# Kernel optimization log

Hardware: AMD Instinct MI355X
Metric: run time of the kernel (lower is better)

## Reference

```python
import jax, jax.numpy as jnp
import numpy as np

D_MODEL, D_STATE, D_CONV, D_INNER = 1024, 16, 4, 2048
BATCH, SEQ = 4, 2048


def silu(v):
    return v * jax.nn.sigmoid(v)


def setup_inputs() -> dict:
    key = jax.random.key(0)
    ks = jax.random.split(key, 7)
    x = jax.random.normal(ks[0], (BATCH, SEQ, D_MODEL), dtype=jnp.float32)
    s = 0.02
    W_in = jax.random.normal(ks[1], (D_MODEL, 2 * D_INNER), dtype=jnp.float32) * s
    conv_w = jax.random.normal(ks[2], (D_INNER, 1, D_CONV), dtype=jnp.float32) * s  # depthwise (O, I/g=1, K)
    conv_b = jax.random.normal(ks[3], (D_INNER,), dtype=jnp.float32) * s
    W_xproj = jax.random.normal(ks[4], (D_INNER, 2 * D_STATE + 1), dtype=jnp.float32) * s
    A_log = jnp.log(jnp.tile(jnp.arange(1, D_STATE + 1, dtype=jnp.float32), (D_INNER, 1)))
    D = jnp.ones((D_INNER,), dtype=jnp.float32)
    W_out = jax.random.normal(ks[5], (D_INNER, D_MODEL), dtype=jnp.float32) * s
    return {"x": x, "W_in": W_in, "conv_w": conv_w, "conv_b": conv_b,
            "W_xproj": W_xproj, "A_log": A_log, "D": D, "W_out": W_out}


def reference(x, W_in, conv_w, conv_b, W_xproj, A_log, D, W_out):
    B, L, _ = x.shape
    xz = x @ W_in                                   # (B, L, 2*d_inner)
    x_proj, z = jnp.split(xz, 2, axis=-1)
    # Depthwise causal conv: padding=d_conv-1 then truncate to L == left-pad only.
    xc = jax.lax.conv_general_dilated(
        x_proj.transpose(0, 2, 1), conv_w,
        window_strides=(1,), padding=[(D_CONV - 1, 0)],
        feature_group_count=D_INNER,
        dimension_numbers=("NCH", "OIH", "NCH"))
    x_conv = silu((xc + conv_b[None, :, None]).transpose(0, 2, 1))  # (B, L, d_inner)
    ssm = x_conv @ W_xproj                           # (B, L, 1+2*d_state)
    delta = jax.nn.softplus(ssm[..., 0])             # (B, L)
    Bm = ssm[..., 1:1 + D_STATE]                     # (B, L, d_state)
    Cm = ssm[..., 1 + D_STATE:]                      # (B, L, d_state)
    # Original: deltaA = exp(delta*A) and softmax weights are computed but unused.
    deltaB = delta[..., None] * Bm                   # (B, L, d_state)
    # h_approx = mean_L(x outer deltaB): avoid (B,L,d_inner,d_state) intermediate.
    h_mean = jnp.einsum("bld,bln->bdn", x_conv, deltaB) / L  # (B, d_inner, d_state)
    y = jnp.einsum("bdn,bln->bld", h_mean, Cm)       # (B, L, d_inner)
    y = y + D[None, None, :] * x_conv
    y = y * silu(z)
    return y @ W_out                                 # (B, L, d_model)
```

## Files before the change

### kernel.cpp

```cpp
#include <hip/hip_runtime.h>
#include <hip/hip_bf16.h>
#include <stdint.h>

typedef __bf16 bf16x8 __attribute__((ext_vector_type(8)));
typedef float f32x4 __attribute__((ext_vector_type(4)));
typedef float f32x2 __attribute__((ext_vector_type(2)));
typedef unsigned short u16;
typedef u16 ushort2v __attribute__((ext_vector_type(2)));
typedef u16 ushort4v __attribute__((ext_vector_type(4)));
typedef u16 ushort8v __attribute__((ext_vector_type(8)));

__device__ __forceinline__ u16 f2bf(float f) {
    union { float f; uint32_t u; } v; v.f = f;
    uint32_t u = v.u + 0x7FFFu + ((v.u >> 16) & 1u);
    return (u16)(u >> 16);
}
__device__ __forceinline__ float bf2f(u16 b) {
    union { uint32_t u; float f; } v; v.u = ((uint32_t)b) << 16;
    return v.f;
}
__device__ __forceinline__ float silu_f(float v) {
    return v / (1.0f + __expf(-v));
}
__device__ __forceinline__ void gload_lds16(const u16* g, u16* l) {
    __builtin_amdgcn_global_load_lds(
        (const __attribute__((address_space(1))) void*)g,
        (__attribute__((address_space(3))) void*)l, 16, 0, 0);
}

__device__ __forceinline__ void trans_tile(
        const float* __restrict__ src, u16* __restrict__ dst, int R, int C,
        int bc, int br, float (*tt)[33], int tid) {
    const int tx = tid & 31, ty = tid >> 5;
#pragma unroll
    for (int i = 0; i < 4; i++)
        tt[ty + i * 8][tx] = src[(int64_t)(br * 32 + ty + i * 8) * C + bc * 32 + tx];
    __syncthreads();
    const int wx = tid & 15, wy = tid >> 4;
#pragma unroll
    for (int i = 0; i < 2; i++) {
        int c = wy + i * 16;
        ushort2v o = { f2bf(tt[wx * 2][c]), f2bf(tt[wx * 2 + 1][c]) };
        *(ushort2v*)&dst[(int64_t)(bc * 32 + c) * R + br * 32 + wx * 2] = o;
    }
}

__global__ __launch_bounds__(256) void prep_k(
        const float* __restrict__ x, u16* __restrict__ x_bf,
        const float* __restrict__ Wi, u16* __restrict__ Wti,
        const float* __restrict__ Wo, u16* __restrict__ Wto,
        const float* __restrict__ wx, u16* __restrict__ wxt) {
    __shared__ float tt[32][33];
    const int blk = blockIdx.x, tid = threadIdx.x;
    if (blk < 4096) {
        int64_t i = ((int64_t)blk * 256 + tid) * 8;
        float4 v0 = *(const float4*)&x[i];
        float4 v1 = *(const float4*)&x[i + 4];
        ushort8v o = { f2bf(v0.x), f2bf(v0.y), f2bf(v0.z), f2bf(v0.w),
                       f2bf(v1.x), f2bf(v1.y), f2bf(v1.z), f2bf(v1.w) };
        *(ushort8v*)&x_bf[i] = o;
    } else if (blk < 8192) {
        int t = blk - 4096;
        trans_tile(Wi, Wti, 1024, 4096, t & 127, t >> 7, tt, tid);
    } else if (blk < 10240) {
        int t = blk - 8192;
        trans_tile(Wo, Wto, 2048, 1024, t & 31, t >> 5, tt, tid);
    } else {
        int idx = (blk - 10240) * 256 + tid;
        int j = idx >> 11, d = idx & 2047;
        wxt[idx] = (j < 33) ? f2bf(wx[d * 33 + j]) : (u16)0;
    }
}

template<int M_REP, int WARPS_M, int B_HALVES, bool OUT_BF16>
__global__ __launch_bounds__(512) void gemm_dp(
        const u16* __restrict__ A, const u16* __restrict__ Bt,
        void* __restrict__ Cout, int nbn_sh, int NT, int lda, int ldb, int ldc) {
    constexpr int WARPS_N = 8 / WARPS_M;
    constexpr int QPT = M_REP / 2;
    constexpr int WV_M = M_REP * 16;
    constexpr int BN = WARPS_N * 64;
    constexpr int B_T = BN * 64;

    __shared__ __align__(16) u16 As[2 * 16384];
    __shared__ __align__(16) u16 Bs[2 * B_T];

    const int tid = threadIdx.x;
    const int wave = tid >> 6;
    const int lane = tid & 63;
    const int wm = wave / WARPS_N, wn = wave % WARPS_N;
    const int fr = lane & 15, fq = lane >> 4;

    const int nwg = gridDim.x;
    const int cpx = nwg >> 3;
    const int swz = (blockIdx.x & 7) * cpx + (blockIdx.x >> 3);
    const int bm = swz >> nbn_sh;
    const int bn = swz & ((1 << nbn_sh) - 1);

    const int srow = tid >> 3;
    const int scol8 = ((tid & 7) ^ (srow & 7)) * 8;
    const u16* gA = A + (int64_t)(bm * 256 + srow) * lda + scol8;
    const u16* gB = Bt + (int64_t)(bn * BN + srow) * ldb + scol8;
    const int64_t lda64 = lda, ldb64 = ldb;

    const int ksw0 = ((fq) ^ (fr & 7)) * 8;
    const int ksw1 = ((4 + fq) ^ (fr & 7)) * 8;
    const int arow0 = (wm * WV_M + fr) * 64;
    const int brow0 = (wn * 64 + fr) * 64;

    auto STAGE_A_HALF = [&](int kt, int buf, int h) {
#pragma unroll
        for (int j = 0; j < 2; ++j)
            gload_lds16(gA + (int64_t)(h * 128 + j * 64) * lda64 + kt * 64,
                        &As[buf * 16384 + h * 8192 + j * 4096 + tid * 8]);
    };
    auto STAGE_B_HALF = [&](int kt, int buf, int h) {
#pragma unroll
        for (int j = 0; j < 2; ++j)
            gload_lds16(gB + (int64_t)(h * 128 + j * 64) * ldb64 + kt * 64,
                        &Bs[buf * B_T + h * 8192 + j * 4096 + tid * 8]);
    };

    f32x4 acc[M_REP][4] = {};

    STAGE_A_HALF(0, 0, 0); STAGE_A_HALF(0, 0, 1);
#pragma unroll
    for (int h = 0; h < B_HALVES; ++h) STAGE_B_HALF(0, 0, h);
#pragma unroll
    for (int h = 0; h < B_HALVES; ++h) STAGE_B_HALF(1, 1, h);
    if constexpr (B_HALVES == 2) { asm volatile("s_waitcnt vmcnt(4)" ::: "memory"); }
    else                         { asm volatile("s_waitcnt vmcnt(2)" ::: "memory"); }
    __builtin_amdgcn_s_barrier();

    const int NI = NT >> 1;
    for (int s = 0; s < NI; ++s) {
        const bool more = (s + 1 < NI);
#pragma unroll
        for (int t = 0; t < 2; ++t) {
            const u16* Ab = &As[t * 16384];
            const u16* Bb = &Bs[t * B_T];
            bf16x8 breg[4][2];
            bf16x8 areg[2][2][2];
#pragma unroll
            for (int q = 0; q < QPT; ++q) {
                const int p = q & 1;
                if (q == 0) {
#pragma unroll
                    for (int n = 0; n < 4; ++n) {
                        breg[n][0] = *(const bf16x8*)(Bb + brow0 + n * 1024 + ksw0);
                        breg[n][1] = *(const bf16x8*)(Bb + brow0 + n * 1024 + ksw1);
                    }
#pragma unroll
                    for (int j = 0; j < 2; ++j) {
                        areg[0][j][0] = *(const bf16x8*)(Ab + arow0 + j * 1024 + ksw0);
                        areg[0][j][1] = *(const bf16x8*)(Ab + arow0 + j * 1024 + ksw1);
                    }
                }
                __builtin_amdgcn_s_setprio(1);
                if (q + 1 < QPT) {
#pragma unroll
                    for (int j = 0; j < 2; ++j) {
                        areg[p ^ 1][j][0] = *(const bf16x8*)(Ab + arow0 + (2 * (q + 1) + j) * 1024 + ksw0);
                        areg[p ^ 1][j][1] = *(const bf16x8*)(Ab + arow0 + (2 * (q + 1) + j) * 1024 + ksw1);
                    }
                }
#pragma unroll
                for (int j = 0; j < 2; ++j)
#pragma unroll
                    for (int n = 0; n < 4; ++n) {
                        acc[2 * q + j][n] = __builtin_amdgcn_mfma_f32_16x16x32_bf16(
                            areg[p][j][0], breg[n][0], acc[2 * q + j][n], 0, 0, 0);
                        acc[2 * q + j][n] = __builtin_amdgcn_mfma_f32_16x16x32_bf16(
                            areg[p][j][1], breg[n][1], acc[2 * q + j][n], 0, 0, 0);
                    }
                if (q + 1 < QPT) {
#pragma unroll
                    for (int g = 0; g < 4; ++g) {
                        __builtin_amdgcn_sched_group_barrier(0x008, 2, 0);
                        __builtin_amdgcn_sched_group_barrier(0x100, 1, 0);
                        __builtin_amdgcn_sched_group_barrier(0x008, 2, 0);
                    }
                }
                __builtin_amdgcn_s_setprio(0);
                if constexpr (QPT == 4) {
                    if (t == 0 && q == 0)         STAGE_A_HALF(2 * s + 1, 1, 0);
                    if (t == 0 && q == 1)         STAGE_A_HALF(2 * s + 1, 1, 1);
                    if (t == 0 && q == 2 && more) STAGE_B_HALF(2 * s + 2, 0, 0);
                    if (t == 0 && q == 3 && more) STAGE_B_HALF(2 * s + 2, 0, 1);
                    if (t == 1 && q == 0 && more) STAGE_A_HALF(2 * s + 2, 0, 0);
                    if (t == 1 && q == 1 && more) STAGE_A_HALF(2 * s + 2, 0, 1);
                    if (t == 1 && q == 2 && more) STAGE_B_HALF(2 * s + 3, 1, 0);
                    if (t == 1 && q == 3 && more) STAGE_B_HALF(2 * s + 3, 1, 1);
                } else {
                    if (t == 0 && q == 0)         STAGE_A_HALF(2 * s + 1, 1, 0);
                    if (t == 0 && q == 1) {       STAGE_A_HALF(2 * s + 1, 1, 1);
                        if (more)                 STAGE_B_HALF(2 * s + 2, 0, 0); }
                    if (t == 1 && q == 0 && more) STAGE_A_HALF(2 * s + 2, 0, 0);
                    if (t == 1 && q == 1 && more) { STAGE_A_HALF(2 * s + 2, 0, 1);
                                                    STAGE_B_HALF(2 * s + 3, 1, 0); }
                }
                if (q == QPT - 1) {
                    if (more) {
                        if constexpr (B_HALVES == 2) { asm volatile("s_waitcnt vmcnt(4)" ::: "memory"); }
                        else                         { asm volatile("s_waitcnt vmcnt(2)" ::: "memory"); }
                    } else {
                        asm volatile("s_waitcnt vmcnt(0)" ::: "memory");
                    }
                }
                __builtin_amdgcn_s_barrier();
            }
        }
    }

#pragma unroll
    for (int m = 0; m < M_REP; ++m) {
#pragma unroll
        for (int n = 0; n < 4; ++n) {
            const int col = bn * BN + wn * 64 + n * 16 + fr;
#pragma unroll
            for (int r = 0; r < 4; ++r) {
                const int row = bm * 256 + wm * WV_M + m * 16 + fq * 4 + r;
                if constexpr (OUT_BF16)
                    ((u16*)Cout)[(int64_t)row * ldc + col] = f2bf(acc[m][n][r]);
                else
                    ((float*)Cout)[(int64_t)row * ldc + col] = acc[m][n][r];
            }
        }
    }
}

__global__ __launch_bounds__(256) void gemm3_k(
        const u16* __restrict__ A, const u16* __restrict__ Bt,
        float* __restrict__ Cout, int NT, int lda, int ldb, int ldc) {
    __shared__ __align__(16) u16 As[2 * 8192];
    __shared__ __align__(16) u16 Bs[2 * 8192];

    const int tid = threadIdx.x;
    const int wave = tid >> 6;
    const int lane = tid & 63;
    const int wm = wave >> 1, wn = wave & 1;
    const int fr = lane & 15, fq = lane >> 4;

    const int nwg = gridDim.x;
    const int cpx = nwg >> 3;
    const int swz = (blockIdx.x & 7) * cpx + (blockIdx.x >> 3);
    const int bm = swz >> 3;
    const int bn = swz & 7;

    const int srow = tid >> 3;
    const int scol8 = ((tid & 7) ^ (srow & 7)) * 8;
    const u16* gA = A + (int64_t)(bm * 128 + srow) * lda + scol8;
    const u16* gB = Bt + (int64_t)(bn * 128 + srow) * ldb + scol8;
    const int64_t lda64 = lda, ldb64 = ldb;

    const int ksw0 = ((fq) ^ (fr & 7)) * 8;
    const int ksw1 = ((4 + fq) ^ (fr & 7)) * 8;
    const int arow0 = (wm * 64 + fr) * 64;
    const int brow0 = (wn * 64 + fr) * 64;

    auto STAGE_A = [&](int kt, int buf, int h) {
#pragma unroll
        for (int j = 0; j < 2; ++j)
            gload_lds16(gA + (int64_t)(h * 64 + j * 32) * lda64 + kt * 64,
                        &As[buf * 8192 + h * 4096 + j * 2048 + tid * 8]);
    };
    auto STAGE_B = [&](int kt, int buf, int h) {
#pragma unroll
        for (int j = 0; j < 2; ++j)
            gload_lds16(gB + (int64_t)(h * 64 + j * 32) * ldb64 + kt * 64,
                        &Bs[buf * 8192 + h * 4096 + j * 2048 + tid * 8]);
    };

    f32x4 acc[4][4] = {};

    STAGE_A(0, 0, 0); STAGE_A(0, 0, 1);
    STAGE_B(0, 0, 0); STAGE_B(0, 0, 1);
    STAGE_B(1, 1, 0); STAGE_B(1, 1, 1);
    asm volatile("s_waitcnt vmcnt(4)" ::: "memory");
    __builtin_amdgcn_s_barrier();

    for (int t = 0; t < NT; ++t) {
        const u16* Ab = &As[(t & 1) * 8192];
        const u16* Bb = &Bs[(t & 1) * 8192];
        bf16x8 breg[4][2];
        bf16x8 areg[2][2][2];
#pragma unroll
        for (int n = 0; n < 4; ++n) {
            breg[n][0] = *(const bf16x8*)(Bb + brow0 + n * 1024 + ksw0);
            breg[n][1] = *(const bf16x8*)(Bb + brow0 + n * 1024 + ksw1);
        }
#pragma unroll
        for (int j = 0; j < 2; ++j) {
            areg[0][j][0] = *(const bf16x8*)(Ab + arow0 + j * 1024 + ksw0);
            areg[0][j][1] = *(const bf16x8*)(Ab + arow0 + j * 1024 + ksw1);
        }
        if (t + 1 < NT) STAGE_A(t + 1, (t + 1) & 1, 0);
        __builtin_amdgcn_s_barrier();
        asm volatile("s_waitcnt lgkmcnt(0)" ::: "memory");
        __builtin_amdgcn_sched_barrier(0);
        __builtin_amdgcn_s_setprio(1);
#pragma unroll
        for (int j = 0; j < 2; ++j) {
            areg[1][j][0] = *(const bf16x8*)(Ab + arow0 + (2 + j) * 1024 + ksw0);
            areg[1][j][1] = *(const bf16x8*)(Ab + arow0 + (2 + j) * 1024 + ksw1);
        }
#pragma unroll
        for (int j = 0; j < 2; ++j)
#pragma unroll
            for (int n = 0; n < 4; ++n) {
                acc[j][n] = __builtin_amdgcn_mfma_f32_16x16x32_bf16(
                    areg[0][j][0], breg[n][0], acc[j][n], 0, 0, 0);
                acc[j][n] = __builtin_amdgcn_mfma_f32_16x16x32_bf16(
                    areg[0][j][1], breg[n][1], acc[j][n], 0, 0, 0);
            }
#pragma unroll
        for (int g = 0; g < 4; ++g) {
            __builtin_amdgcn_sched_group_barrier(0x008, 2, 0);
            __builtin_amdgcn_sched_group_barrier(0x100, 1, 0);
            __builtin_amdgcn_sched_group_barrier(0x008, 2, 0);
        }
        __builtin_amdgcn_s_setprio(0);
        __builtin_amdgcn_s_barrier();
        if (t + 1 < NT) STAGE_A(t + 1, (t + 1) & 1, 1);
        if (t + 2 < NT) { STAGE_B(t + 2, t & 1, 0); STAGE_B(t + 2, t & 1, 1); }
        __builtin_amdgcn_s_barrier();
        asm volatile("s_waitcnt lgkmcnt(0)" ::: "memory");
        __builtin_amdgcn_sched_barrier(0);
        __builtin_amdgcn_s_setprio(1);
#pragma unroll
        for (int j = 0; j < 2; ++j)
#pragma unroll
            for (int n = 0; n < 4; ++n) {
                acc[2 + j][n] = __builtin_amdgcn_mfma_f32_16x16x32_bf16(
                    areg[1][j][0], breg[n][0], acc[2 + j][n], 0, 0, 0);
                acc[2 + j][n] = __builtin_amdgcn_mfma_f32_16x16x32_bf16(
                    areg[1][j][1], breg[n][1], acc[2 + j][n], 0, 0, 0);
            }
        __builtin_amdgcn_s_setprio(0);
        if (t + 2 < NT) { asm volatile("s_waitcnt vmcnt(4)" ::: "memory"); }
        else            { asm volatile("s_waitcnt vmcnt(0)" ::: "memory"); }
        __builtin_amdgcn_s_barrier();
    }

#pragma unroll
    for (int m = 0; m < 4; ++m) {
#pragma unroll
        for (int n = 0; n < 4; ++n) {
            const int col = bn * 128 + wn * 64 + n * 16 + fr;
#pragma unroll
            for (int r = 0; r < 4; ++r) {
                const int row = bm * 128 + wm * 64 + m * 16 + fq * 4 + r;
                Cout[(int64_t)row * ldc + col] = acc[m][n][r];
            }
        }
    }
}

__global__ __launch_bounds__(256) void conv_ssm_k(
        const u16* __restrict__ xz, const float* __restrict__ cw,
        const float* __restrict__ cb, const u16* __restrict__ wxt,
        u16* __restrict__ xc, float* __restrict__ dB, float* __restrict__ Cm) {
    __shared__ __align__(16) u16 Xs[16][2064];
    __shared__ float Sred[4][16][48];
    __shared__ float deltas[16];
    const int blk = blockIdx.x;
    const int b = blk >> 7, lb = blk & 127;
    const int l0 = lb << 4;
    const int64_t r0 = (int64_t)b * 2048 + l0;
    const int tid = threadIdx.x;
    const int d0 = tid * 8;

    float w[8][4], bias[8];
#pragma unroll
    for (int j = 0; j < 8; j++) {
        float4 wv = *(const float4*)&cw[(d0 + j) * 4];
        w[j][0] = wv.x; w[j][1] = wv.y; w[j][2] = wv.z; w[j][3] = wv.w;
        bias[j] = cb[d0 + j];
    }
    float win[4][8];
#pragma unroll
    for (int r = 0; r < 3; r++) {
        int l = l0 - 3 + r;
        if (l < 0) {
#pragma unroll
            for (int j = 0; j < 8; j++) win[r][j] = 0.f;
        } else {
            ushort8v v = *(const ushort8v*)&xz[((int64_t)b * 2048 + l) * 4096 + d0];
#pragma unroll
            for (int j = 0; j < 8; j++) win[r][j] = bf2f(v[j]);
        }
    }
    ushort8v rows[16];
#pragma unroll
    for (int li = 0; li < 16; li++)
        rows[li] = *(const ushort8v*)&xz[(r0 + li) * 4096 + d0];

#pragma unroll
    for (int li = 0; li < 16; li++) {
#pragma unroll
        for (int j = 0; j < 8; j++) win[(3 + li) & 3][j] = bf2f(rows[li][j]);
        ushort8v o;
#pragma unroll
        for (int j = 0; j < 8; j++) {
            float s = bias[j];
#pragma unroll
            for (int k = 0; k < 4; k++) s += w[j][k] * win[(li + k) & 3][j];
            o[j] = f2bf(silu_f(s));
        }
        *(ushort8v*)&xc[(r0 + li) * 2048 + d0] = o;
        *(ushort8v*)&Xs[li][d0] = o;
    }
    __syncthreads();

    const int kc = tid >> 6;
    const int lane = tid & 63;
    const int fr = lane & 15, fq = lane >> 4;
    const u16* bp = wxt + (int64_t)fr * 2048 + kc * 512 + fq * 8;
    const u16* ap = &Xs[fr][kc * 512 + fq * 8];
    f32x4 acc0 = {}, acc1 = {}, acc2 = {};
#pragma unroll 4
    for (int k = 0; k < 512; k += 32) {
        bf16x8 av = *(const bf16x8*)(ap + k);
        bf16x8 b0 = *(const bf16x8*)(bp + k);
        bf16x8 b1 = *(const bf16x8*)(bp + 16 * 2048 + k);
        bf16x8 b2 = *(const bf16x8*)(bp + 32 * 2048 + k);
        acc0 = __builtin_amdgcn_mfma_f32_16x16x32_bf16(av, b0, acc0, 0, 0, 0);
        acc1 = __builtin_amdgcn_mfma_f32_16x16x32_bf16(av, b1, acc1, 0, 0, 0);
        acc2 = __builtin_amdgcn_mfma_f32_16x16x32_bf16(av, b2, acc2, 0, 0, 0);
    }
#pragma unroll
    for (int r = 0; r < 4; r++) {
        Sred[kc][fq * 4 + r][fr]      = acc0[r];
        Sred[kc][fq * 4 + r][16 + fr] = acc1[r];
        Sred[kc][fq * 4 + r][32 + fr] = acc2[r];
    }
    __syncthreads();
    if (tid < 16) {
        float s0 = Sred[0][tid][0] + Sred[1][tid][0] + Sred[2][tid][0] + Sred[3][tid][0];
        deltas[tid] = (s0 > 20.f) ? s0 : log1pf(__expf(s0));
    }
    __syncthreads();
    {
        const int row = tid >> 4, n = tid & 15;
        float sB = Sred[0][row][1 + n] + Sred[1][row][1 + n] +
                   Sred[2][row][1 + n] + Sred[3][row][1 + n];
        float sC = Sred[0][row][17 + n] + Sred[1][row][17 + n] +
                   Sred[2][row][17 + n] + Sred[3][row][17 + n];
        dB[(r0 + row) * 16 + n] = deltas[row] * sB * (1.0f / 2048.0f);
        Cm[(r0 + row) * 16 + n] = sC;
    }
}

__global__ __launch_bounds__(256) void h_part_k(
        const u16* __restrict__ xc, const float* __restrict__ dB,
        float* __restrict__ hp) {
    const int blk = blockIdx.x;
    const int dt = blk & 3, b = (blk >> 2) & 3, lc = blk >> 4;
    const int d = dt * 512 + threadIdx.x * 2;
    const u16* xp = xc + ((int64_t)(b * 2048 + lc * 64)) * 2048 + d;
    const f32x2* dbp = (const f32x2*)(dB + (int64_t)(b * 2048 + lc * 64) * 16);
    f32x2 acc0[8] = {}, acc1[8] = {};
    for (int l = 0; l < 64; l++) {
        ushort2v xv = *(const ushort2v*)&xp[(int64_t)l * 2048];
        float x0 = bf2f(xv[0]), x1 = bf2f(xv[1]);
#pragma unroll
        for (int q = 0; q < 8; q++) {
            f32x2 dv = dbp[l * 8 + q];
            acc0[q] += dv * x0;
            acc1[q] += dv * x1;
        }
    }
    float* o = hp + ((int64_t)((lc * 4 + b) * 2048 + d)) * 16;
#pragma unroll
    for (int q = 0; q < 8; q++) *(f32x2*)&o[q * 2] = acc0[q];
#pragma unroll
    for (int q = 0; q < 8; q++) *(f32x2*)&o[16 + q * 2] = acc1[q];
}

__global__ void h_red_k(const float* __restrict__ hp, float* __restrict__ h) {
    const int i4 = blockIdx.x * 256 + threadIdx.x;
    f32x4 s = {};
#pragma unroll
    for (int c = 0; c < 32; c++)
        s += *(const f32x4*)&hp[(int64_t)c * 131072 + i4 * 4];
    *(f32x4*)&h[i4 * 4] = s;
}

__global__ __launch_bounds__(256) void y_gate_k(
        u16* __restrict__ xz, const u16* __restrict__ xc,
        const float* __restrict__ h, const float* __restrict__ Cm,
        const float* __restrict__ Dp) {
    const int blk = blockIdx.x;
    const int lc = blk & 127, b = blk >> 7;
    const int d0 = threadIdx.x * 8;
    const float* hpp = h + ((int64_t)(b * 2048 + d0)) * 16;
    float hreg[8][16];
#pragma unroll
    for (int i = 0; i < 8; i++)
#pragma unroll
        for (int n4 = 0; n4 < 4; n4++) {
            f32x4 hv = *(const f32x4*)&hpp[i * 16 + n4 * 4];
            hreg[i][n4 * 4 + 0] = hv[0]; hreg[i][n4 * 4 + 1] = hv[1];
            hreg[i][n4 * 4 + 2] = hv[2]; hreg[i][n4 * 4 + 3] = hv[3];
        }
    float Dv[8];
    {
        f32x4 dv0 = *(const f32x4*)&Dp[d0];
        f32x4 dv1 = *(const f32x4*)&Dp[d0 + 4];
#pragma unroll
        for (int i = 0; i < 4; i++) { Dv[i] = dv0[i]; Dv[4 + i] = dv1[i]; }
    }
    __shared__ float Cs[16][16];
    if (threadIdx.x < 64)
        ((float4*)&Cs[0][0])[threadIdx.x] =
            ((const float4*)(Cm + (int64_t)(b * 2048 + lc * 16) * 16))[threadIdx.x];
    __syncthreads();
#pragma unroll 4
    for (int li = 0; li < 16; li++) {
        const int64_t rowz = (int64_t)(b * 2048 + lc * 16 + li);
        ushort8v xcv = *(const ushort8v*)&xc[rowz * 2048 + d0];
        ushort8v zv = *(const ushort8v*)&xz[rowz * 4096 + 2048 + d0];
        ushort8v o;
#pragma unroll
        for (int i = 0; i < 8; i++) {
            float s = Dv[i] * bf2f(xcv[i]);
#pragma unroll
            for (int n = 0; n < 16; n++) s += hreg[i][n] * Cs[li][n];
            o[i] = f2bf(s * silu_f(bf2f(zv[i])));
        }
        *(ushort8v*)&xz[rowz * 4096 + d0] = o;
    }
}

extern "C" void kernel_launch(void* const* d_in, const int* in_sizes, int n_in,
                              void* d_out, int out_size, void* d_ws, size_t ws_size,
                              hipStream_t stream) {
    (void)in_sizes; (void)n_in; (void)out_size; (void)ws_size;
    const float* x      = (const float*)d_in[0];
    const float* W_in   = (const float*)d_in[1];
    const float* conv_w = (const float*)d_in[2];
    const float* conv_b = (const float*)d_in[3];
    const float* W_xp   = (const float*)d_in[4];
    const float* Dp     = (const float*)d_in[6];
    const float* W_out  = (const float*)d_in[7];
    float* out = (float*)d_out;
    char* ws = (char*)d_ws;

    u16*   x_bf   = (u16*)(ws);
    float* dB     = (float*)(ws);
    float* Cm     = (float*)(ws + 524288);
    float* h      = (float*)(ws + 1048576);
    float* hp     = (float*)(ws + 1572864);
    u16*   Wt_in  = (u16*)(ws + 16777216);
    u16*   Wt_out = (u16*)(ws + 25165824);
    u16*   Wxt    = (u16*)(ws + 29360128);
    u16*   xz     = (u16*)(ws + 29556736);
    u16*   xcv    = (u16*)(ws + 96665600);

    prep_k<<<10624, 256, 0, stream>>>(x, x_bf, W_in, Wt_in, W_out, Wt_out, W_xp, Wxt);
    gemm_dp<8, 2, 2, true><<<512, 512, 0, stream>>>(x_bf, Wt_in, xz, 4, 16, 1024, 1024, 4096);
    conv_ssm_k<<<512, 256, 0, stream>>>(xz, conv_w, conv_b, Wxt, xcv, dB, Cm);
    h_part_k<<<512, 256, 0, stream>>>(xcv, dB, hp);
    h_red_k<<<128, 256, 0, stream>>>(hp, h);
    y_gate_k<<<512, 256, 0, stream>>>(xz, xcv, h, Cm, Dp);
    gemm3_k<<<512, 256, 0, stream>>>(xz, Wt_out, out, 32, 4096, 2048, 1024);
}
```

Before: 205.1 us.

## Switch input-projection GEMM to 32x32x16 MFMA tiles with 2x4 wave layout

Replaces the templated 16x16x32 MFMA GEMM for the input projection with a dedicated kernel using 32x32x16 bf16 MFMAs. Each wave now computes a 128x64 tile (4x2 of 32x32 fragments) under a 2x4 wave grid, with the LDS read pattern, swizzle offsets and store mapping reworked to match. The aim is fewer LDS reads per flop and higher MFMA throughput per instruction. The finer sched_group_barrier interleaving is dropped and staging is regrouped into whole-tile chunks, which may reduce overlap between LDS reads and MFMAs.

```diff
diff --git a/kernel.cpp b/kernel.cpp
--- a/kernel.cpp
+++ b/kernel.cpp
@@ -5,6 +5,7 @@
 typedef __bf16 bf16x8 __attribute__((ext_vector_type(8)));
 typedef float f32x4 __attribute__((ext_vector_type(4)));
 typedef float f32x2 __attribute__((ext_vector_type(2)));
+typedef float f32x16 __attribute__((ext_vector_type(16)));
 typedef unsigned short u16;
 typedef u16 ushort2v __attribute__((ext_vector_type(2)));
 typedef u16 ushort4v __attribute__((ext_vector_type(4)));
@@ -72,24 +73,19 @@
     }
 }
 
-template<int M_REP, int WARPS_M, int B_HALVES, bool OUT_BF16>
-__global__ __launch_bounds__(512) void gemm_dp(
+__global__ __launch_bounds__(512) void gemm1_k(
         const u16* __restrict__ A, const u16* __restrict__ Bt,
-        void* __restrict__ Cout, int nbn_sh, int NT, int lda, int ldb, int ldc) {
-    constexpr int WARPS_N = 8 / WARPS_M;
-    constexpr int QPT = M_REP / 2;
-    constexpr int WV_M = M_REP * 16;
-    constexpr int BN = WARPS_N * 64;
-    constexpr int B_T = BN * 64;
-
+        u16* __restrict__ Cout, int nbn_sh, int NT, int lda, int ldb, int ldc) {
     __shared__ __align__(16) u16 As[2 * 16384];
-    __shared__ __align__(16) u16 Bs[2 * B_T];
+    __shared__ __align__(16) u16 Bs[2 * 16384];
 
     const int tid = threadIdx.x;
     const int wave = tid >> 6;
     const int lane = tid & 63;
-    const int wm = wave / WARPS_N, wn = wave % WARPS_N;
-    const int fr = lane & 15, fq = lane >> 4;
+    const int wm = wave >> 2, wn = wave & 3;
+    const int r32 = lane & 31;
+    const int kh = lane >> 5;
+    const int l7 = lane & 7;
 
     const int nwg = gridDim.x;
     const int cpx = nwg >> 3;
@@ -100,13 +96,8 @@
     const int srow = tid >> 3;
     const int scol8 = ((tid & 7) ^ (srow & 7)) * 8;
     const u16* gA = A + (int64_t)(bm * 256 + srow) * lda + scol8;
-    const u16* gB = Bt + (int64_t)(bn * BN + srow) * ldb + scol8;
+    const u16* gB = Bt + (int64_t)(bn * 256 + srow) * ldb + scol8;
     const int64_t lda64 = lda, ldb64 = ldb;
-
-    const int ksw0 = ((fq) ^ (fr & 7)) * 8;
-    const int ksw1 = ((4 + fq) ^ (fr & 7)) * 8;
-    const int arow0 = (wm * WV_M + fr) * 64;
-    const int brow0 = (wn * 64 + fr) * 64;
 
     auto STAGE_A_HALF = [&](int kt, int buf, int h) {
 #pragma unroll
@@ -118,18 +109,21 @@
 #pragma unroll
         for (int j = 0; j < 2; ++j)
             gload_lds16(gB + (int64_t)(h * 128 + j * 64) * ldb64 + kt * 64,
-                        &Bs[buf * B_T + h * 8192 + j * 4096 + tid * 8]);
+                        &Bs[buf * 16384 + h * 8192 + j * 4096 + tid * 8]);
     };
-
-    f32x4 acc[M_REP][4] = {};
+    int ksl[4];
+#pragma unroll
+    for (int ks = 0; ks < 4; ++ks) ksl[ks] = ((ks * 2 + kh) ^ l7) * 8;
+    const int arow[4] = { (wm * 128 + 0 * 32 + r32) * 64, (wm * 128 + 1 * 32 + r32) * 64,
+                          (wm * 128 + 2 * 32 + r32) * 64, (wm * 128 + 3 * 32 + r32) * 64 };
+    const int brow[2] = { (wn * 64 + 0 * 32 + r32) * 64, (wn * 64 + 1 * 32 + r32) * 64 };
+
+    f32x16 acc[4][2] = {};
 
     STAGE_A_HALF(0, 0, 0); STAGE_A_HALF(0, 0, 1);
-#pragma unroll
-    for (int h = 0; h < B_HALVES; ++h) STAGE_B_HALF(0, 0, h);
-#pragma unroll
-    for (int h = 0; h < B_HALVES; ++h) STAGE_B_HALF(1, 1, h);
-    if constexpr (B_HALVES == 2) { asm volatile("s_waitcnt vmcnt(4)" ::: "memory"); }
-    else                         { asm volatile("s_waitcnt vmcnt(2)" ::: "memory"); }
+    STAGE_B_HALF(0, 0, 0); STAGE_B_HALF(0, 0, 1);
+    STAGE_B_HALF(1, 1, 0); STAGE_B_HALF(1, 1, 1);
+    asm volatile("s_waitcnt vmcnt(4)" ::: "memory");
     __builtin_amdgcn_s_barrier();
 
     const int NI = NT >> 1;
@@ -138,74 +132,44 @@
 #pragma unroll
         for (int t = 0; t < 2; ++t) {
             const u16* Ab = &As[t * 16384];
-            const u16* Bb = &Bs[t * B_T];
-            bf16x8 breg[4][2];
-            bf16x8 areg[2][2][2];
-#pragma unroll
-            for (int q = 0; q < QPT; ++q) {
-                const int p = q & 1;
+            const u16* Bb = &Bs[t * 16384];
+            bf16x8 breg[2][4];
+#pragma unroll
+            for (int q = 0; q < 2; ++q) {
+                bf16x8 areg[2][4];
                 if (q == 0) {
 #pragma unroll
-                    for (int n = 0; n < 4; ++n) {
-                        breg[n][0] = *(const bf16x8*)(Bb + brow0 + n * 1024 + ksw0);
-                        breg[n][1] = *(const bf16x8*)(Bb + brow0 + n * 1024 + ksw1);
-                    }
-#pragma unroll
-                    for (int j = 0; j < 2; ++j) {
-                        areg[0][j][0] = *(const bf16x8*)(Ab + arow0 + j * 1024 + ksw0);
-                        areg[0][j][1] = *(const bf16x8*)(Ab + arow0 + j * 1024 + ksw1);
-                    }
+                    for (int nt = 0; nt < 2; ++nt)
+#pragma unroll
+                        for (int ks = 0; ks < 4; ++ks)
+                            breg[nt][ks] = *(const bf16x8*)(Bb + brow[nt] + ksl[ks]);
                 }
+#pragma unroll
+                for (int j = 0; j < 2; ++j)
+#pragma unroll
+                    for (int ks = 0; ks < 4; ++ks)
+                        areg[j][ks] = *(const bf16x8*)(Ab + arow[2 * q + j] + ksl[ks]);
                 __builtin_amdgcn_s_setprio(1);
-                if (q + 1 < QPT) {
-#pragma unroll
-                    for (int j = 0; j < 2; ++j) {
-                        areg[p ^ 1][j][0] = *(const bf16x8*)(Ab + arow0 + (2 * (q + 1) + j) * 1024 + ksw0);
-                        areg[p ^ 1][j][1] = *(const bf16x8*)(Ab + arow0 + (2 * (q + 1) + j) * 1024 + ksw1);
-                    }
-                }
 #pragma unroll
                 for (int j = 0; j < 2; ++j)
 #pragma unroll
-                    for (int n = 0; n < 4; ++n) {
-                        acc[2 * q + j][n] = __builtin_amdgcn_mfma_f32_16x16x32_bf16(
-                            areg[p][j][0], breg[n][0], acc[2 * q + j][n], 0, 0, 0);
-                        acc[2 * q + j][n] = __builtin_amdgcn_mfma_f32_16x16x32_bf16(
-                            areg[p][j][1], breg[n][1], acc[2 * q + j][n], 0, 0, 0);
-                    }
-                if (q + 1 < QPT) {
-#pragma unroll
-                    for (int g = 0; g < 4; ++g) {
-                        __builtin_amdgcn_sched_group_barrier(0x008, 2, 0);
-                        __builtin_amdgcn_sched_group_barrier(0x100, 1, 0);
-                        __builtin_amdgcn_sched_group_barrier(0x008, 2, 0);
-                    }
-                }
+                    for (int nt = 0; nt < 2; ++nt)
+#pragma unroll
+                        for (int ks = 0; ks < 4; ++ks)
+                            acc[2 * q + j][nt] = __builtin_amdgcn_mfma_f32_32x32x16_bf16(
+                                areg[j][ks], breg[nt][ks], acc[2 * q + j][nt], 0, 0, 0);
                 __builtin_amdgcn_s_setprio(0);
-                if constexpr (QPT == 4) {
-                    if (t == 0 && q == 0)         STAGE_A_HALF(2 * s + 1, 1, 0);
-                    if (t == 0 && q == 1)         STAGE_A_HALF(2 * s + 1, 1, 1);
-                    if (t == 0 && q == 2 && more) STAGE_B_HALF(2 * s + 2, 0, 0);
-                    if (t == 0 && q == 3 && more) STAGE_B_HALF(2 * s + 2, 0, 1);
-                    if (t == 1 && q == 0 && more) STAGE_A_HALF(2 * s + 2, 0, 0);
-                    if (t == 1 && q == 1 && more) STAGE_A_HALF(2 * s + 2, 0, 1);
-                    if (t == 1 && q == 2 && more) STAGE_B_HALF(2 * s + 3, 1, 0);
-                    if (t == 1 && q == 3 && more) STAGE_B_HALF(2 * s + 3, 1, 1);
-                } else {
-                    if (t == 0 && q == 0)         STAGE_A_HALF(2 * s + 1, 1, 0);
-                    if (t == 0 && q == 1) {       STAGE_A_HALF(2 * s + 1, 1, 1);
-                        if (more)                 STAGE_B_HALF(2 * s + 2, 0, 0); }
-                    if (t == 1 && q == 0 && more) STAGE_A_HALF(2 * s + 2, 0, 0);
-                    if (t == 1 && q == 1 && more) { STAGE_A_HALF(2 * s + 2, 0, 1);
-                                                    STAGE_B_HALF(2 * s + 3, 1, 0); }
-                }
-                if (q == QPT - 1) {
-                    if (more) {
-                        if constexpr (B_HALVES == 2) { asm volatile("s_waitcnt vmcnt(4)" ::: "memory"); }
-                        else                         { asm volatile("s_waitcnt vmcnt(2)" ::: "memory"); }
-                    } else {
-                        asm volatile("s_waitcnt vmcnt(0)" ::: "memory");
-                    }
+                if (t == 0 && q == 0) { STAGE_A_HALF(2 * s + 1, 1, 0);
+                                        STAGE_A_HALF(2 * s + 1, 1, 1); }
+                if (t == 0 && q == 1 && more) { STAGE_B_HALF(2 * s + 2, 0, 0);
+                                                STAGE_B_HALF(2 * s + 2, 0, 1); }
+                if (t == 1 && q == 0 && more) { STAGE_A_HALF(2 * s + 2, 0, 0);
+                                                STAGE_A_HALF(2 * s + 2, 0, 1); }
+                if (t == 1 && q == 1 && more) { STAGE_B_HALF(2 * s + 3, 1, 0);
+                                                STAGE_B_HALF(2 * s + 3, 1, 1); }
+                if (q == 1) {
+                    if (more) { asm volatile("s_waitcnt vmcnt(4)" ::: "memory"); }
+                    else      { asm volatile("s_waitcnt vmcnt(0)" ::: "memory"); }
                 }
                 __builtin_amdgcn_s_barrier();
             }
@@ -213,17 +177,15 @@
     }
 
 #pragma unroll
-    for (int m = 0; m < M_REP; ++m) {
-#pragma unroll
-        for (int n = 0; n < 4; ++n) {
-            const int col = bn * BN + wn * 64 + n * 16 + fr;
-#pragma unroll
-            for (int r = 0; r < 4; ++r) {
-                const int row = bm * 256 + wm * WV_M + m * 16 + fq * 4 + r;
-                if constexpr (OUT_BF16)
-                    ((u16*)Cout)[(int64_t)row * ldc + col] = f2bf(acc[m][n][r]);
-                else
-                    ((float*)Cout)[(int64_t)row * ldc + col] = acc[m][n][r];
+    for (int mt = 0; mt < 4; ++mt) {
+#pragma unroll
+        for (int nt = 0; nt < 2; ++nt) {
+            const int col = bn * 256 + wn * 64 + nt * 32 + r32;
+#pragma unroll
+            for (int reg = 0; reg < 16; ++reg) {
+                const int row = bm * 256 + wm * 128 + mt * 32 +
+                                (reg & 3) + 8 * (reg >> 2) + 4 * kh;
+                Cout[(int64_t)row * ldc + col] = f2bf(acc[mt][nt][reg]);
             }
         }
     }
@@ -558,7 +520,7 @@
     u16*   xcv    = (u16*)(ws + 96665600);
 
     prep_k<<<10624, 256, 0, stream>>>(x, x_bf, W_in, Wt_in, W_out, Wt_out, W_xp, Wxt);
-    gemm_dp<8, 2, 2, true><<<512, 512, 0, stream>>>(x_bf, Wt_in, xz, 4, 16, 1024, 1024, 4096);
+    gemm1_k<<<512, 512, 0, stream>>>(x_bf, Wt_in, xz, 4, 16, 1024, 1024, 4096);
     conv_ssm_k<<<512, 256, 0, stream>>>(xz, conv_w, conv_b, Wxt, xcv, dB, Cm);
     h_part_k<<<512, 256, 0, stream>>>(xcv, dB, hp);
     h_red_k<<<128, 256, 0, stream>>>(hp, h);
```

Measured after the change: 210.9 us. +2.8%, slower.

## Fuse h partial, reduction and gating kernels into one cooperative kernel

Applied to the files above, without the earlier changes.

Replaces the three separate launches (h partial sums, h reduction, y gating) with a single cooperative kernel that uses grid-wide syncs between the phases. This removes two kernel launch boundaries and their drain and refill gaps. In exchange it adds grid.sync overhead and requires all 512 blocks to be co-resident, with a fallback to the old kernels if the cooperative launch fails.

```diff
diff --git a/kernel.cpp b/kernel.cpp
--- a/kernel.cpp
+++ b/kernel.cpp
@@ -1,6 +1,9 @@
 #include <hip/hip_runtime.h>
 #include <hip/hip_bf16.h>
+#include <hip/hip_cooperative_groups.h>
 #include <stdint.h>
+
+namespace cg = cooperative_groups;
 
 typedef __bf16 bf16x8 __attribute__((ext_vector_type(8)));
 typedef float f32x4 __attribute__((ext_vector_type(4)));
@@ -532,6 +535,94 @@
     }
 }
 
+__global__ __launch_bounds__(256, 2) void fused_tail_k(
+        u16* __restrict__ xz, const u16* __restrict__ xc,
+        const float* __restrict__ dB, const float* __restrict__ Cm,
+        float* __restrict__ hp, float* __restrict__ h,
+        const float* __restrict__ Dp) {
+    cg::grid_group grid = cg::this_grid();
+    __shared__ float Cs[16][16];
+    const int tid = threadIdx.x;
+    const int bid = blockIdx.x;
+
+    {
+        const int dt = bid & 3, b = (bid >> 2) & 3, lc = bid >> 4;
+        const int d = dt * 512 + tid * 2;
+        const u16* xp = xc + ((int64_t)(b * 2048 + lc * 64)) * 2048 + d;
+        const f32x2* dbp = (const f32x2*)(dB + (int64_t)(b * 2048 + lc * 64) * 16);
+        f32x2 acc0[8] = {}, acc1[8] = {};
+        for (int l = 0; l < 64; l++) {
+            ushort2v xv = *(const ushort2v*)&xp[(int64_t)l * 2048];
+            float x0 = bf2f(xv[0]), x1 = bf2f(xv[1]);
+#pragma unroll
+            for (int q = 0; q < 8; q++) {
+                f32x2 dv = dbp[l * 8 + q];
+                acc0[q] += dv * x0;
+                acc1[q] += dv * x1;
+            }
+        }
+        float* o = hp + ((int64_t)((lc * 4 + b) * 2048 + d)) * 16;
+#pragma unroll
+        for (int q = 0; q < 8; q++) *(f32x2*)&o[q * 2] = acc0[q];
+#pragma unroll
+        for (int q = 0; q < 8; q++) *(f32x2*)&o[16 + q * 2] = acc1[q];
+    }
+    __threadfence();
+    grid.sync();
+
+    if (bid < 128) {
+        const int i4 = bid * 256 + tid;
+        f32x4 s = {};
+#pragma unroll
+        for (int c = 0; c < 32; c++)
+            s += *(const f32x4*)&hp[(int64_t)c * 131072 + i4 * 4];
+        *(f32x4*)&h[i4 * 4] = s;
+    }
+    __threadfence();
+    grid.sync();
+
+    {
+        const int lc = bid & 127, b = bid >> 7;
+        const int d0 = tid * 8;
+        const float* hpp = h + ((int64_t)(b * 2048 + d0)) * 16;
+        float hreg[8][16];
+#pragma unroll
+        for (int i = 0; i < 8; i++)
+#pragma unroll
+            for (int n4 = 0; n4 < 4; n4++) {
+                f32x4 hv = *(const f32x4*)&hpp[i * 16 + n4 * 4];
+                hreg[i][n4 * 4 + 0] = hv[0]; hreg[i][n4 * 4 + 1] = hv[1];
+                hreg[i][n4 * 4 + 2] = hv[2]; hreg[i][n4 * 4 + 3] = hv[3];
+            }
+        float Dv[8];
+        {
+            f32x4 dv0 = *(const f32x4*)&Dp[d0];
+            f32x4 dv1 = *(const f32x4*)&Dp[d0 + 4];
+#pragma unroll
+            for (int i = 0; i < 4; i++) { Dv[i] = dv0[i]; Dv[4 + i] = dv1[i]; }
+        }
+        if (tid < 64)
+            ((float4*)&Cs[0][0])[tid] =
+                ((const float4*)(Cm + (int64_t)(b * 2048 + lc * 16) * 16))[tid];
+        __syncthreads();
+#pragma unroll 4
+        for (int li = 0; li < 16; li++) {
+            const int64_t rowz = (int64_t)(b * 2048 + lc * 16 + li);
+            ushort8v xcv = *(const ushort8v*)&xc[rowz * 2048 + d0];
+            ushort8v zv = *(const ushort8v*)&xz[rowz * 4096 + 2048 + d0];
+            ushort8v o;
+#pragma unroll
+            for (int i = 0; i < 8; i++) {
+                float s = Dv[i] * bf2f(xcv[i]);
+#pragma unroll
+                for (int n = 0; n < 16; n++) s += hreg[i][n] * Cs[li][n];
+                o[i] = f2bf(s * silu_f(bf2f(zv[i])));
+            }
+            *(ushort8v*)&xz[rowz * 4096 + d0] = o;
+        }
+    }
+}
+
 extern "C" void kernel_launch(void* const* d_in, const int* in_sizes, int n_in,
                               void* d_out, int out_size, void* d_ws, size_t ws_size,
                               hipStream_t stream) {
@@ -560,8 +651,16 @@
     prep_k<<<10624, 256, 0, stream>>>(x, x_bf, W_in, Wt_in, W_out, Wt_out, W_xp, Wxt);
     gemm_dp<8, 2, 2, true><<<512, 512, 0, stream>>>(x_bf, Wt_in, xz, 4, 16, 1024, 1024, 4096);
     conv_ssm_k<<<512, 256, 0, stream>>>(xz, conv_w, conv_b, Wxt, xcv, dB, Cm);
-    h_part_k<<<512, 256, 0, stream>>>(xcv, dB, hp);
-    h_red_k<<<128, 256, 0, stream>>>(hp, h);
-    y_gate_k<<<512, 256, 0, stream>>>(xz, xcv, h, Cm, Dp);
+    {
+        void* args[] = { &xz, &xcv, &dB, &Cm, &hp, &h, &Dp };
+        hipError_t ce = hipLaunchCooperativeKernel((void*)fused_tail_k,
+                                                   dim3(512), dim3(256),
+                                                   args, 0, stream);
+        if (ce != hipSuccess) {
+            h_part_k<<<512, 256, 0, stream>>>(xcv, dB, hp);
+            h_red_k<<<128, 256, 0, stream>>>(hp, h);
+            y_gate_k<<<512, 256, 0, stream>>>(xz, xcv, h, Cm, Dp);
+        }
+    }
     gemm3_k<<<512, 256, 0, stream>>>(xz, Wt_out, out, 32, 4096, 2048, 1024);
 }
```

Measured after the change: 431.8 us. 111% more time.
